# Kernel optimization log

Hardware: AMD Instinct MI355X
Metric: run time of the kernel (lower is better)

The kernel has to match this reference:

```python
import jax, jax.numpy as jnp
import numpy as np

B, T, H, M = 16, 1024, 512, 80
NHEADS, HDIM = 8, H // 8


def _p(key, shape, scale=0.05):
    return scale * jax.random.normal(key, shape, dtype=jnp.float32)


def setup_inputs() -> dict:
    key = jax.random.key(0)
    ks = jax.random.split(key, 20)
    return {
        "encoder_memory": jax.random.normal(ks[0], (B, T, H), dtype=jnp.float32),
        "target_mel": jax.random.normal(ks[1], (B, T, M), dtype=jnp.float32),
        # prenet Linear(mel_dim -> hidden_dim)
        "w_prenet": _p(ks[2], (H, M)), "b_prenet": _p(ks[3], (H,)),
        # MultiheadAttention packed in-proj (3H, H) and out-proj (H, H)
        "in_proj_w": _p(ks[4], (3 * H, H)), "in_proj_b": _p(ks[5], (3 * H,)),
        "out_proj_w": _p(ks[6], (H, H)), "out_proj_b": _p(ks[7], (H,)),
        # 2-layer LSTM (torch gate order i,f,g,o); h0=c0=0 each step so W_hh acts on zeros
        "w_ih0": _p(ks[8], (4 * H, 2 * H)), "w_hh0": _p(ks[9], (4 * H, H)),
        "b_ih0": _p(ks[10], (4 * H,)), "b_hh0": _p(ks[11], (4 * H,)),
        "w_ih1": _p(ks[12], (4 * H, H)), "w_hh1": _p(ks[13], (4 * H, H)),
        "b_ih1": _p(ks[14], (4 * H,)), "b_hh1": _p(ks[15], (4 * H,)),
        # mel projection Linear(hidden_dim -> mel_dim)
        "w_mel": _p(ks[16], (M, H)), "b_mel": _p(ks[17], (M,)),
    }


def _lstm_cell_zero_state(x, w_ih, w_hh, b_ih, b_hh):
    # single step from zero (h, c): the W_hh @ h0 term is exactly zero
    gates = x @ w_ih.T + (b_ih + b_hh)  # (B,T,4H)
    i, f, g, o = jnp.split(gates, 4, axis=-1)
    c = jax.nn.sigmoid(i) * jnp.tanh(g)  # f * c_prev == 0
    return jax.nn.sigmoid(o) * jnp.tanh(c)


def reference(encoder_memory, target_mel, w_prenet, b_prenet,
              in_proj_w, in_proj_b, out_proj_w, out_proj_b,
              w_ih0, w_hh0, b_ih0, b_hh0, w_ih1, w_hh1, b_ih1, b_hh1,
              w_mel, b_mel):
    # teacher forcing: prev_mel at step t is zeros (t=0) else target_mel[:, t-1]
    prev = jnp.concatenate(
        [jnp.zeros((B, 1, M), dtype=target_mel.dtype), target_mel[:, :-1]], axis=1)
    pre = jax.nn.relu(prev @ w_prenet.T + b_prenet)  # (B,T,H); dropout is identity (eval)

    # cross-attention: each step's length-1 query attends over all encoder frames,
    # which vectorizes to standard (no-mask) MHA with queries = pre
    wq, wk, wv = jnp.split(in_proj_w, 3, axis=0)
    bq, bk, bv = jnp.split(in_proj_b, 3, axis=0)
    q = (pre @ wq.T + bq).reshape(B, T, NHEADS, HDIM)
    k = (encoder_memory @ wk.T + bk).reshape(B, T, NHEADS, HDIM)
    v = (encoder_memory @ wv.T + bv).reshape(B, T, NHEADS, HDIM)
    scale = 1.0 / jnp.sqrt(jnp.float32(HDIM))
    scores = jnp.einsum('bqhd,bkhd->bhqk', q * scale, k)  # (B,8,T,T)
    attn = jax.nn.softmax(scores, axis=-1)
    ctx = jnp.einsum('bhqk,bkhd->bqhd', attn, v).reshape(B, T, H)
    attn_out = ctx @ out_proj_w.T + out_proj_b  # (B,T,H)

    dec_in = jnp.concatenate([pre, attn_out], axis=-1)  # (B,T,2H)
    h1 = _lstm_cell_zero_state(dec_in, w_ih0, w_hh0, b_ih0, b_hh0)
    h2 = _lstm_cell_zero_state(h1, w_ih1, w_hh1, b_ih1, b_hh1)
    return h2 @ w_mel.T + b_mel  # (B,T,M)
```

## Files before the change

### kernel.cpp

```cpp
#include <hip/hip_runtime.h>


typedef _Float16 f16;
typedef _Float16 f16x8 __attribute__((ext_vector_type(8)));
typedef _Float16 f16x4 __attribute__((ext_vector_type(4)));
typedef float f32x4 __attribute__((ext_vector_type(4)));

constexpr int B_ = 16, T_ = 1024, H_ = 512, M_ = 80;
constexpr int NH_ = 8, D_ = 64;
constexpr int N_ = B_ * T_;

#define MFMA16(a, b, c) __builtin_amdgcn_mfma_f32_16x16x32_f16(a, b, c, 0, 0, 0)

__device__ __forceinline__ void gload_lds16(const f16* g, f16* l) {
  __builtin_amdgcn_global_load_lds(
      (const __attribute__((address_space(1))) void*)g,
      (__attribute__((address_space(3))) void*)l, 16, 0, 0);
}

template <int EPI, bool CONCATA, bool NCHK>
__global__ __launch_bounds__(256) void mgemm(
    const f16* __restrict__ A, const f16* __restrict__ A2,
    const f16* __restrict__ Wt, const float* __restrict__ bias,
    const float* __restrict__ bias2, float scale, void* __restrict__ outp,
    int K, int N) {
  __shared__ f16 As[128 * 64];
  __shared__ f16 Bs[128 * 64];
  const int tid = threadIdx.x;
  const int lane = tid & 63, wid = tid >> 6;
  const int lq = lane & 15, lg = lane >> 4;
  const int wm = wid >> 1, wn = wid & 1;
  const int r0 = blockIdx.x * 128, c0 = blockIdx.y * 128;

  f32x4 acc[4][4] = {};

  for (int k0 = 0; k0 < K; k0 += 64) {
#pragma unroll
    for (int it = 0; it < 4; ++it) {
      const int off = it * 4096 + wid * 1024 + lane * 16;
      const int row = off >> 7;
      const int cb = (off >> 4) & 7;
      const int kc = k0 + ((cb ^ (row & 7)) << 3);
      const f16* src;
      if (CONCATA) {
        src = (kc < 512) ? (A + (size_t)(r0 + row) * 512 + kc)
                         : (A2 + (size_t)(r0 + row) * 512 + (kc - 512));
      } else {
        src = A + (size_t)(r0 + row) * K + kc;
      }
      gload_lds16(src, (f16*)((char*)As + off));
    }
#pragma unroll
    for (int it = 0; it < 4; ++it) {
      const int off = it * 4096 + wid * 1024 + lane * 16;
      const int row = off >> 7;
      const int cb = (off >> 4) & 7;
      int crow = c0 + row;
      if (NCHK) crow = crow < N ? crow : N - 1;
      gload_lds16(Wt + (size_t)crow * K + k0 + ((cb ^ (row & 7)) << 3),
                  (f16*)((char*)Bs + off));
    }
    __syncthreads();
#pragma unroll
    for (int kk = 0; kk < 2; ++kk) {
      f16x8 af[4], bf[4];
#pragma unroll
      for (int m = 0; m < 4; ++m) {
        const int row = wm * 64 + m * 16 + lq;
        af[m] = *(const f16x8*)((const char*)As + row * 128 +
                                (((kk * 4 + lg) ^ (row & 7)) << 4));
      }
#pragma unroll
      for (int n = 0; n < 4; ++n) {
        const int row = wn * 64 + n * 16 + lq;
        bf[n] = *(const f16x8*)((const char*)Bs + row * 128 +
                                (((kk * 4 + lg) ^ (row & 7)) << 4));
      }
#pragma unroll
      for (int m = 0; m < 4; ++m)
#pragma unroll
        for (int n = 0; n < 4; ++n) acc[m][n] = MFMA16(af[m], bf[n], acc[m][n]);
    }
    __syncthreads();
  }

#pragma unroll
  for (int m = 0; m < 4; ++m) {
    const int rbase = r0 + wm * 64 + m * 16 + lg * 4;
#pragma unroll
    for (int n = 0; n < 4; ++n) {
      const int col = c0 + wn * 64 + n * 16 + lq;
      if (NCHK && col >= N) continue;
      const float bsum = bias[col] + (bias2 ? bias2[col] : 0.f);
      const f32x4 a = acc[m][n];
      if (EPI == 3) {
        const int b = rbase >> 10, t = rbase & (T_ - 1);
        const int head = col >> 6, d = col & 63;
        f16x4 pk;
#pragma unroll
        for (int r = 0; r < 4; ++r) pk[r] = (f16)((a[r] + bsum) * scale);
        *(f16x4*)((f16*)outp + ((size_t)((b * NH_ + head) * D_ + d)) * T_ + t) =
            pk;
      } else {
#pragma unroll
        for (int r = 0; r < 4; ++r) {
          const int row = rbase + r;
          float v = (a[r] + bsum) * scale;
          if (EPI == 1) v = fmaxf(v, 0.f);
          if (EPI == 4)
            ((float*)outp)[(size_t)row * N + col] = v;
          else
            ((f16*)outp)[(size_t)row * N + col] = (f16)v;
        }
      }
    }
  }
}

template <bool CONCATA>
__global__ __launch_bounds__(256, 2) void lstm_fused(
    const f16* __restrict__ A, const f16* __restrict__ A2,
    const f16* __restrict__ Wih, const float* __restrict__ bih,
    const float* __restrict__ bhh, f16* __restrict__ Hout_) {
  constexpr int K = CONCATA ? 1024 : 512;
  __shared__ f16 As[128 * 64];
  __shared__ f16 Bs[3][128 * 64];
  const int tid = threadIdx.x;
  const int lane = tid & 63, wid = tid >> 6;
  const int lq = lane & 15, lg = lane >> 4;
  const int wm = wid >> 1, wn = wid & 1;
  const int r0 = blockIdx.x * 128, c0 = blockIdx.y * 128;

  f32x4 acc[3][4][4] = {};

  for (int k0 = 0; k0 < K; k0 += 64) {
#pragma unroll
    for (int it = 0; it < 4; ++it) {
      const int off = it * 4096 + tid * 16;
      const int row = off >> 7;
      const int cb = (off >> 4) & 7;
      const int kc = k0 + ((cb ^ (row & 7)) << 3);
      const f16* src;
      if (CONCATA) {
        src = (kc < 512) ? (A + (size_t)(r0 + row) * 512 + kc)
                         : (A2 + (size_t)(r0 + row) * 512 + (kc - 512));
      } else {
        src = A + (size_t)(r0 + row) * K + kc;
      }
      gload_lds16(src, (f16*)((char*)As + off));
    }
#pragma unroll
    for (int g = 0; g < 3; ++g) {
      const int gbase = (g == 0) ? 0 : 512 * (g + 1);
#pragma unroll
      for (int it = 0; it < 4; ++it) {
        const int off = it * 4096 + tid * 16;
        const int row = off >> 7;
        const int cb = (off >> 4) & 7;
        gload_lds16(
            Wih + (size_t)(gbase + c0 + row) * K + k0 + ((cb ^ (row & 7)) << 3),
            (f16*)((char*)&Bs[g][0] + off));
      }
    }
    __syncthreads();
#pragma unroll
    for (int kk = 0; kk < 2; ++kk) {
      f16x8 af[4];
#pragma unroll
      for (int m = 0; m < 4; ++m) {
        const int row = wm * 64 + m * 16 + lq;
        af[m] = *(const f16x8*)((const char*)As + row * 128 +
                                (((kk * 4 + lg) ^ (row & 7)) << 4));
      }
#pragma unroll
      for (int g = 0; g < 3; ++g)
#pragma unroll
        for (int n = 0; n < 4; ++n) {
          const int row = wn * 64 + n * 16 + lq;
          const f16x8 bf = *(const f16x8*)((const char*)&Bs[g][0] + row * 128 +
                                           (((kk * 4 + lg) ^ (row & 7)) << 4));
#pragma unroll
          for (int m = 0; m < 4; ++m)
            acc[g][m][n] = MFMA16(af[m], bf, acc[g][m][n]);
        }
    }
    __syncthreads();
  }

#pragma unroll
  for (int n = 0; n < 4; ++n) {
    const int c = c0 + wn * 64 + n * 16 + lq;
    const float bi = bih[c] + bhh[c];
    const float bg = bih[1024 + c] + bhh[1024 + c];
    const float bo = bih[1536 + c] + bhh[1536 + c];
#pragma unroll
    for (int m = 0; m < 4; ++m) {
      const int rbase = r0 + wm * 64 + m * 16 + lg * 4;
#pragma unroll
      for (int r = 0; r < 4; ++r) {
        const float gi = acc[0][m][n][r] + bi;
        const float gg = acc[1][m][n][r] + bg;
        const float go = acc[2][m][n][r] + bo;
        const float si = 1.f / (1.f + __expf(-gi));
        const float so = 1.f / (1.f + __expf(-go));
        const float tg = 2.f / (1.f + __expf(-2.f * gg)) - 1.f;
        const float cc = si * tg;
        const float tc = 2.f / (1.f + __expf(-2.f * cc)) - 1.f;
        Hout_[(size_t)(rbase + r) * 512 + c] = (f16)(so * tc);
      }
    }
  }
}

__global__ __launch_bounds__(256, 2) void kv_fused(
    const f16* __restrict__ A, const f16* __restrict__ Wt,
    const float* __restrict__ bias, f16* __restrict__ kout,
    f16* __restrict__ vout) {
  constexpr int K = 512;
  __shared__ f16 As[128 * 64];
  __shared__ f16 Bs[2][128 * 64];
  const int tid = threadIdx.x;
  const int lane = tid & 63, wid = tid >> 6;
  const int lq = lane & 15, lg = lane >> 4;
  const int wm = wid >> 1, wn = wid & 1;
  const int r0 = blockIdx.x * 128, c0 = blockIdx.y * 128;

  f32x4 acc[2][4][4] = {};

  for (int k0 = 0; k0 < K; k0 += 64) {
#pragma unroll
    for (int it = 0; it < 4; ++it) {
      const int off = it * 4096 + tid * 16;
      const int row = off >> 7;
      const int cb = (off >> 4) & 7;
      const int kc = k0 + ((cb ^ (row & 7)) << 3);
      gload_lds16(A + (size_t)(r0 + row) * K + kc, (f16*)((char*)As + off));
    }
#pragma unroll
    for (int g = 0; g < 2; ++g) {
#pragma unroll
      for (int it = 0; it < 4; ++it) {
        const int off = it * 4096 + tid * 16;
        const int row = off >> 7;
        const int cb = (off >> 4) & 7;
        gload_lds16(
            Wt + (size_t)(g * 512 + c0 + row) * K + k0 + ((cb ^ (row & 7)) << 3),
            (f16*)((char*)&Bs[g][0] + off));
      }
    }
    __syncthreads();
#pragma unroll
    for (int kk = 0; kk < 2; ++kk) {
      f16x8 af[4];
#pragma unroll
      for (int m = 0; m < 4; ++m) {
        const int row = wm * 64 + m * 16 + lq;
        af[m] = *(const f16x8*)((const char*)As + row * 128 +
                                (((kk * 4 + lg) ^ (row & 7)) << 4));
      }
#pragma unroll
      for (int g = 0; g < 2; ++g)
#pragma unroll
        for (int n = 0; n < 4; ++n) {
          const int row = wn * 64 + n * 16 + lq;
          const f16x8 bf = *(const f16x8*)((const char*)&Bs[g][0] + row * 128 +
                                           (((kk * 4 + lg) ^ (row & 7)) << 4));
#pragma unroll
          for (int m = 0; m < 4; ++m)
            acc[g][m][n] = MFMA16(af[m], bf, acc[g][m][n]);
        }
    }
    __syncthreads();
  }

#pragma unroll
  for (int m = 0; m < 4; ++m) {
    const int rbase = r0 + wm * 64 + m * 16 + lg * 4;
    const int b = rbase >> 10, t = rbase & (T_ - 1);
#pragma unroll
    for (int n = 0; n < 4; ++n) {
      const int col = c0 + wn * 64 + n * 16 + lq;
      const float bk = bias[col];
#pragma unroll
      for (int r = 0; r < 4; ++r)
        kout[(size_t)(rbase + r) * 512 + col] = (f16)(acc[0][m][n][r] + bk);
      const float bv = bias[512 + col];
      const int head = col >> 6, d = col & 63;
      f16x4 pk;
#pragma unroll
      for (int r = 0; r < 4; ++r) pk[r] = (f16)(acc[1][m][n][r] + bv);
      *(f16x4*)(vout + ((size_t)((b * NH_ + head) * D_ + d)) * T_ + t) = pk;
    }
  }
}

__global__ __launch_bounds__(256) void attn_mfma3(
    const f16* __restrict__ q, const f16* __restrict__ k,
    const f16* __restrict__ vT, f16* __restrict__ ctx) {
  __shared__ f16 Ks[2][64 * 64];
  __shared__ f16 Vs[2][64 * 64];
  __shared__ f16 Ps[4][16 * 64];
  const int qt = blockIdx.x, head = blockIdx.y, b = blockIdx.z;
  const int tid = threadIdx.x, lane = tid & 63, wid = tid >> 6;
  const int lq = lane & 15, lg = lane >> 4;
  const int bh = b * NH_ + head;

  const f16* kbase = k + ((size_t)b * T_) * H_ + head * D_;
  const f16* vbase = vT + (size_t)bh * D_ * T_;

  auto stage = [&](int kt, int buf) {
#pragma unroll
    for (int it = 0; it < 2; ++it) {
      const int off = it * 4096 + tid * 16;
      const int row = off >> 7;
      const int sc = ((((off >> 4) & 7) ^ (row & 7)) << 3);
      gload_lds16(kbase + (size_t)(kt * 64 + row) * H_ + sc,
                  (f16*)((char*)&Ks[buf][0] + off));
      gload_lds16(vbase + (size_t)row * T_ + kt * 64 + sc,
                  (f16*)((char*)&Vs[buf][0] + off));
    }
  };

  const int q0 = qt * 128 + wid * 32;
  f16x8 qf[2][2];
#pragma unroll
  for (int s = 0; s < 2; ++s)
#pragma unroll
    for (int kk = 0; kk < 2; ++kk)
      qf[s][kk] = *(const f16x8*)(q + ((size_t)(b * T_) + q0 + s * 16 + lq) * H_ +
                                  head * D_ + kk * 32 + lg * 8);

  float m_run[2] = {-1e30f, -1e30f}, l_run[2] = {0.f, 0.f};
  f32x4 accO[2][4] = {};
  char* pw = (char*)&Ps[wid][0] + lq * 128;
  const int psw = (lq & 3) << 5;

  stage(0, 0);
  __syncthreads();

  for (int kt = 0; kt < T_ / 64; ++kt) {
    const int cur = kt & 1;
    if (kt < T_ / 64 - 1) stage(kt + 1, cur ^ 1);

    f16x8 kf[4][2];
#pragma unroll
    for (int n = 0; n < 4; ++n)
#pragma unroll
      for (int kk = 0; kk < 2; ++kk) {
        const int row = n * 16 + lq;
        kf[n][kk] = *(const f16x8*)((const char*)&Ks[cur][0] + row * 128 +
                                    (((kk * 4 + lg) ^ (row & 7)) << 4));
      }
    f32x4 ssw[2][4] = {};
    __builtin_amdgcn_s_setprio(1);
#pragma unroll
    for (int s = 0; s < 2; ++s)
#pragma unroll
      for (int n = 0; n < 4; ++n)
#pragma unroll
        for (int kk = 0; kk < 2; ++kk)
          ssw[s][n] = MFMA16(kf[n][kk], qf[s][kk], ssw[s][n]);
    __builtin_amdgcn_s_setprio(0);

    f16x8 vf[4][2];
#pragma unroll
    for (int n = 0; n < 4; ++n)
#pragma unroll
      for (int kk = 0; kk < 2; ++kk) {
        const int row = n * 16 + lq;
        vf[n][kk] = *(const f16x8*)((const char*)&Vs[cur][0] + row * 128 +
                                    (((kk * 4 + lg) ^ (row & 7)) << 4));
      }

#pragma unroll
    for (int s = 0; s < 2; ++s) {
      float mloc = -1e30f;
#pragma unroll
      for (int n = 0; n < 4; ++n)
#pragma unroll
        for (int r = 0; r < 4; ++r) mloc = fmaxf(mloc, ssw[s][n][r]);
      mloc = fmaxf(mloc, __shfl_xor(mloc, 16, 64));
      mloc = fmaxf(mloc, __shfl_xor(mloc, 32, 64));

      const bool noresc = __all(mloc - m_run[s] <= 8.f);
      if (!noresc) {
        const float nm = fmaxf(m_run[s], mloc);
        const float corr = __expf(m_run[s] - nm);
        m_run[s] = nm;
        l_run[s] *= corr;
#pragma unroll
        for (int n = 0; n < 4; ++n) {
          accO[s][n][0] *= corr; accO[s][n][1] *= corr;
          accO[s][n][2] *= corr; accO[s][n][3] *= corr;
        }
      }
      float sl = 0.f;
#pragma unroll
      for (int n = 0; n < 4; ++n) {
        f16x4 pk;
#pragma unroll
        for (int r = 0; r < 4; ++r) {
          const float p = __expf(ssw[s][n][r] - m_run[s]);
          sl += p;
          pk[r] = (f16)p;
        }
        *(f16x4*)(pw + ((n * 32 + lg * 8) ^ psw)) = pk;
      }
      sl += __shfl_xor(sl, 16, 64);
      sl += __shfl_xor(sl, 32, 64);
      l_run[s] += sl;

      f16x8 pb[2];
#pragma unroll
      for (int kk = 0; kk < 2; ++kk)
        pb[kk] = *(const f16x8*)(pw + ((((kk * 4 + lg) << 4)) ^ psw));
      __builtin_amdgcn_s_setprio(1);
#pragma unroll
      for (int n = 0; n < 4; ++n)
#pragma unroll
        for (int kk = 0; kk < 2; ++kk)
          accO[s][n] = MFMA16(vf[n][kk], pb[kk], accO[s][n]);
      __builtin_amdgcn_s_setprio(0);
    }
    __syncthreads();
  }

#pragma unroll
  for (int s = 0; s < 2; ++s) {
    const float inv = 1.f / l_run[s];
    const size_t rowoff = ((size_t)(b * T_) + q0 + s * 16 + lq) * H_ + head * D_;
#pragma unroll
    for (int n = 0; n < 4; ++n) {
      f16x4 o;
#pragma unroll
      for (int r = 0; r < 4; ++r) o[r] = (f16)(accO[s][n][r] * inv);
      *(f16x4*)(ctx + rowoff + n * 16 + lg * 4) = o;
    }
  }
}

constexpr int C0 = 2097152;
constexpr int C1 = C0 + 196608;
constexpr int C2 = C1 + 65536;
constexpr int C3 = C2 + 524288;
constexpr int C4 = C3 + 262144;
constexpr int C5 = C4 + 10240;
__global__ void conv_all(const float* __restrict__ enc, const float* __restrict__ inw,
                         const float* __restrict__ outw, const float* __restrict__ wih0,
                         const float* __restrict__ wih1, const float* __restrict__ wmel,
                         f16* denc, f16* dinw, f16* doutw, f16* dwih0,
                         f16* dwih1, f16* dwmel) {
  const int i = blockIdx.x * blockDim.x + threadIdx.x;
  const float* s;
  f16* d;
  int off;
  if (i < C0) { s = enc; d = denc; off = i; }
  else if (i < C1) { s = inw; d = dinw; off = i - C0; }
  else if (i < C2) { s = outw; d = doutw; off = i - C1; }
  else if (i < C3) { s = wih0; d = dwih0; off = i - C2; }
  else if (i < C4) { s = wih1; d = dwih1; off = i - C3; }
  else if (i < C5) { s = wmel; d = dwmel; off = i - C4; }
  else return;
  const float4 v = ((const float4*)s)[off];
  f16x4 o = {(f16)v.x, (f16)v.y, (f16)v.z, (f16)v.w};
  ((f16x4*)d)[off] = o;
}

__global__ void build_pm(const float* __restrict__ tmel, f16* __restrict__ pm) {
  const int i = blockIdx.x * blockDim.x + threadIdx.x;
  const int r = i >> 5, c4 = (i & 31) * 4;
  const int t = r & (T_ - 1);
  f16x4 o = {};
  if (t != 0 && c4 < M_) {
    const float4 v = *(const float4*)(tmel + (size_t)(r - 1) * M_ + c4);
    o = {(f16)v.x, (f16)v.y, (f16)v.z, (f16)v.w};
  }
  *(f16x4*)(pm + (size_t)r * 128 + c4) = o;
}

__global__ void build_wp(const float* __restrict__ w, f16* __restrict__ wp) {
  const int i = blockIdx.x * blockDim.x + threadIdx.x;
  const int r = i >> 5, c4 = (i & 31) * 4;
  f16x4 o = {};
  if (c4 < M_) {
    const float4 v = *(const float4*)(w + (size_t)r * M_ + c4);
    o = {(f16)v.x, (f16)v.y, (f16)v.z, (f16)v.w};
  }
  *(f16x4*)(wp + (size_t)r * 128 + c4) = o;
}

extern "C" void kernel_launch(void* const* d_in, const int* in_sizes, int n_in,
                              void* d_out, int out_size, void* d_ws,
                              size_t ws_size, hipStream_t stream) {
  const float* enc = (const float*)d_in[0];
  const float* tmel = (const float*)d_in[1];
  const float* w_pre = (const float*)d_in[2];
  const float* b_pre = (const float*)d_in[3];
  const float* inw = (const float*)d_in[4];
  const float* inb = (const float*)d_in[5];
  const float* outw = (const float*)d_in[6];
  const float* outb = (const float*)d_in[7];
  const float* wih0 = (const float*)d_in[8];
  const float* bih0 = (const float*)d_in[10];
  const float* bhh0 = (const float*)d_in[11];
  const float* wih1 = (const float*)d_in[12];
  const float* bih1 = (const float*)d_in[14];
  const float* bhh1 = (const float*)d_in[15];
  const float* wmel = (const float*)d_in[16];
  const float* bmel = (const float*)d_in[17];

  f16* wsh = (f16*)d_ws;
  const size_t SEG = (size_t)N_ * H_;
  f16* EncB = wsh;
  f16* h1 = wsh + SEG;
  f16* pre = wsh + 2 * SEG;
  f16* qb = wsh + 3 * SEG;
  f16* kbuf = wsh + 4 * SEG;
  f16* vTb = wsh + 5 * SEG;
  f16* ctx = wsh + 6 * SEG;
  f16* aout = EncB;
  f16* h2 = qb;
  f16* WP = wsh + 7 * SEG;
  f16* WIN = WP + 512 * 128;
  f16* WOUT = WIN + 1536 * 512;
  f16* WIH0 = WOUT + 512 * 512;
  f16* WIH1 = WIH0 + 2048 * 1024;
  f16* WMEL = WIH1 + 2048 * 512;
  f16* PM = WMEL + 80 * 512;

  const dim3 blk(256);
  conv_all<<<(C5 + 255) / 256, blk, 0, stream>>>(enc, inw, outw, wih0, wih1,
                                                 wmel, EncB, WIN, WOUT, WIH0,
                                                 WIH1, WMEL);
  build_pm<<<(N_ * 32) / 256, blk, 0, stream>>>(tmel, PM);
  build_wp<<<(512 * 32) / 256, blk, 0, stream>>>(w_pre, WP);

  const dim3 g512(N_ / 128, 4), g80(N_ / 128, 1);
  mgemm<1, false, false><<<g512, blk, 0, stream>>>(PM, nullptr, WP, b_pre,
                                                   nullptr, 1.f, pre, 128, 512);
  mgemm<0, false, false><<<g512, blk, 0, stream>>>(pre, nullptr, WIN, inb,
                                                   nullptr, 0.125f, qb, 512, 512);
  kv_fused<<<g512, blk, 0, stream>>>(EncB, WIN + 512 * 512, inb + 512, kbuf,
                                     vTb);
  attn_mfma3<<<dim3(T_ / 128, NH_, B_), blk, 0, stream>>>(qb, kbuf, vTb, ctx);
  mgemm<0, false, false><<<g512, blk, 0, stream>>>(ctx, nullptr, WOUT, outb,
                                                   nullptr, 1.f, aout, 512, 512);
  lstm_fused<true><<<g512, blk, 0, stream>>>(pre, aout, WIH0, bih0, bhh0, h1);
  lstm_fused<false><<<g512, blk, 0, stream>>>(h1, nullptr, WIH1, bih1, bhh1, h2);
  mgemm<4, false, true><<<g80, blk, 0, stream>>>(h2, nullptr, WMEL, bmel,
                                                 nullptr, 1.f, (float*)d_out,
                                                 512, 80);
}
```

Measured before the change: 285.7 us.

## Enlarge attention query tile, remap blocks for XCD locality, use exp2 softmax

The attention kernel now gives each wave 64 query rows instead of 32, so every block covers 256 queries and each staged K/V tile is reused twice as much. The grid becomes a 1D launch of 512 blocks, remapped so that blocks sharing a (batch, head) land on the same XCD for L2 reuse. The log2(e) factor is folded into the Q projection scale so softmax can use exp2f, and the three input-conversion kernels are merged into one launch. In exchange there are fewer blocks for the GPU, higher register pressure from the larger accumulators, and a change to the P-buffer swizzle.

```diff
diff --git a/kernel.cpp b/kernel.cpp
--- a/kernel.cpp
+++ b/kernel.cpp
@@ -294,16 +294,18 @@
   }
 }
 
-__global__ __launch_bounds__(256) void attn_mfma3(
+__global__ __launch_bounds__(256) void attn_mfma4(
     const f16* __restrict__ q, const f16* __restrict__ k,
     const f16* __restrict__ vT, f16* __restrict__ ctx) {
   __shared__ f16 Ks[2][64 * 64];
   __shared__ f16 Vs[2][64 * 64];
   __shared__ f16 Ps[4][16 * 64];
-  const int qt = blockIdx.x, head = blockIdx.y, b = blockIdx.z;
+  const int bid = blockIdx.x;
+  const int wq = (bid & 7) * 64 + (bid >> 3);
+  const int qt = wq & 3, bh = wq >> 2;
+  const int head = bh & 7, b = bh >> 3;
   const int tid = threadIdx.x, lane = tid & 63, wid = tid >> 6;
   const int lq = lane & 15, lg = lane >> 4;
-  const int bh = b * NH_ + head;
 
   const f16* kbase = k + ((size_t)b * T_) * H_ + head * D_;
   const f16* vbase = vT + (size_t)bh * D_ * T_;
@@ -321,19 +323,20 @@
     }
   };
 
-  const int q0 = qt * 128 + wid * 32;
-  f16x8 qf[2][2];
-#pragma unroll
-  for (int s = 0; s < 2; ++s)
+  const int q0 = qt * 256 + wid * 64;
+  f16x8 qf[4][2];
+#pragma unroll
+  for (int s = 0; s < 4; ++s)
 #pragma unroll
     for (int kk = 0; kk < 2; ++kk)
       qf[s][kk] = *(const f16x8*)(q + ((size_t)(b * T_) + q0 + s * 16 + lq) * H_ +
                                   head * D_ + kk * 32 + lg * 8);
 
-  float m_run[2] = {-1e30f, -1e30f}, l_run[2] = {0.f, 0.f};
-  f32x4 accO[2][4] = {};
+  float m_run[4] = {-1e30f, -1e30f, -1e30f, -1e30f};
+  float l_run[4] = {0.f, 0.f, 0.f, 0.f};
+  f32x4 accO[4][4] = {};
   char* pw = (char*)&Ps[wid][0] + lq * 128;
-  const int psw = (lq & 3) << 5;
+  const int psw = (lq & 7) << 4;
 
   stage(0, 0);
   __syncthreads();
@@ -342,7 +345,7 @@
     const int cur = kt & 1;
     if (kt < T_ / 64 - 1) stage(kt + 1, cur ^ 1);
 
-    f16x8 kf[4][2];
+    f16x8 kf[4][2], vf[4][2];
 #pragma unroll
     for (int n = 0; n < 4; ++n)
 #pragma unroll
@@ -350,42 +353,33 @@
         const int row = n * 16 + lq;
         kf[n][kk] = *(const f16x8*)((const char*)&Ks[cur][0] + row * 128 +
                                     (((kk * 4 + lg) ^ (row & 7)) << 4));
-      }
-    f32x4 ssw[2][4] = {};
-    __builtin_amdgcn_s_setprio(1);
-#pragma unroll
-    for (int s = 0; s < 2; ++s)
-#pragma unroll
-      for (int n = 0; n < 4; ++n)
-#pragma unroll
-        for (int kk = 0; kk < 2; ++kk)
-          ssw[s][n] = MFMA16(kf[n][kk], qf[s][kk], ssw[s][n]);
-    __builtin_amdgcn_s_setprio(0);
-
-    f16x8 vf[4][2];
-#pragma unroll
-    for (int n = 0; n < 4; ++n)
-#pragma unroll
-      for (int kk = 0; kk < 2; ++kk) {
-        const int row = n * 16 + lq;
         vf[n][kk] = *(const f16x8*)((const char*)&Vs[cur][0] + row * 128 +
                                     (((kk * 4 + lg) ^ (row & 7)) << 4));
       }
 
 #pragma unroll
-    for (int s = 0; s < 2; ++s) {
+    for (int s = 0; s < 4; ++s) {
+      f32x4 ssw[4] = {};
+      __builtin_amdgcn_s_setprio(1);
+#pragma unroll
+      for (int n = 0; n < 4; ++n)
+#pragma unroll
+        for (int kk = 0; kk < 2; ++kk)
+          ssw[n] = MFMA16(kf[n][kk], qf[s][kk], ssw[n]);
+      __builtin_amdgcn_s_setprio(0);
+
       float mloc = -1e30f;
 #pragma unroll
       for (int n = 0; n < 4; ++n)
 #pragma unroll
-        for (int r = 0; r < 4; ++r) mloc = fmaxf(mloc, ssw[s][n][r]);
+        for (int r = 0; r < 4; ++r) mloc = fmaxf(mloc, ssw[n][r]);
       mloc = fmaxf(mloc, __shfl_xor(mloc, 16, 64));
       mloc = fmaxf(mloc, __shfl_xor(mloc, 32, 64));
 
       const bool noresc = __all(mloc - m_run[s] <= 8.f);
       if (!noresc) {
         const float nm = fmaxf(m_run[s], mloc);
-        const float corr = __expf(m_run[s] - nm);
+        const float corr = exp2f(m_run[s] - nm);
         m_run[s] = nm;
         l_run[s] *= corr;
 #pragma unroll
@@ -400,7 +394,7 @@
         f16x4 pk;
 #pragma unroll
         for (int r = 0; r < 4; ++r) {
-          const float p = __expf(ssw[s][n][r] - m_run[s]);
+          const float p = exp2f(ssw[n][r] - m_run[s]);
           sl += p;
           pk[r] = (f16)p;
         }
@@ -426,7 +420,7 @@
   }
 
 #pragma unroll
-  for (int s = 0; s < 2; ++s) {
+  for (int s = 0; s < 4; ++s) {
     const float inv = 1.f / l_run[s];
     const size_t rowoff = ((size_t)(b * T_) + q0 + s * 16 + lq) * H_ + head * D_;
 #pragma unroll
@@ -445,48 +439,49 @@
 constexpr int C3 = C2 + 524288;
 constexpr int C4 = C3 + 262144;
 constexpr int C5 = C4 + 10240;
+constexpr int C6 = C5 + 524288;
+constexpr int C7 = C6 + 16384;
 __global__ void conv_all(const float* __restrict__ enc, const float* __restrict__ inw,
                          const float* __restrict__ outw, const float* __restrict__ wih0,
                          const float* __restrict__ wih1, const float* __restrict__ wmel,
+                         const float* __restrict__ tmel, const float* __restrict__ wpre,
                          f16* denc, f16* dinw, f16* doutw, f16* dwih0,
-                         f16* dwih1, f16* dwmel) {
+                         f16* dwih1, f16* dwmel, f16* dpm, f16* dwp) {
   const int i = blockIdx.x * blockDim.x + threadIdx.x;
-  const float* s;
-  f16* d;
-  int off;
-  if (i < C0) { s = enc; d = denc; off = i; }
-  else if (i < C1) { s = inw; d = dinw; off = i - C0; }
-  else if (i < C2) { s = outw; d = doutw; off = i - C1; }
-  else if (i < C3) { s = wih0; d = dwih0; off = i - C2; }
-  else if (i < C4) { s = wih1; d = dwih1; off = i - C3; }
-  else if (i < C5) { s = wmel; d = dwmel; off = i - C4; }
-  else return;
-  const float4 v = ((const float4*)s)[off];
-  f16x4 o = {(f16)v.x, (f16)v.y, (f16)v.z, (f16)v.w};
-  ((f16x4*)d)[off] = o;
-}
-
-__global__ void build_pm(const float* __restrict__ tmel, f16* __restrict__ pm) {
-  const int i = blockIdx.x * blockDim.x + threadIdx.x;
-  const int r = i >> 5, c4 = (i & 31) * 4;
-  const int t = r & (T_ - 1);
-  f16x4 o = {};
-  if (t != 0 && c4 < M_) {
-    const float4 v = *(const float4*)(tmel + (size_t)(r - 1) * M_ + c4);
-    o = {(f16)v.x, (f16)v.y, (f16)v.z, (f16)v.w};
-  }
-  *(f16x4*)(pm + (size_t)r * 128 + c4) = o;
-}
-
-__global__ void build_wp(const float* __restrict__ w, f16* __restrict__ wp) {
-  const int i = blockIdx.x * blockDim.x + threadIdx.x;
-  const int r = i >> 5, c4 = (i & 31) * 4;
-  f16x4 o = {};
-  if (c4 < M_) {
-    const float4 v = *(const float4*)(w + (size_t)r * M_ + c4);
-    o = {(f16)v.x, (f16)v.y, (f16)v.z, (f16)v.w};
-  }
-  *(f16x4*)(wp + (size_t)r * 128 + c4) = o;
+  if (i >= C7) return;
+  if (i < C5) {
+    const float* s;
+    f16* d;
+    int off;
+    if (i < C0) { s = enc; d = denc; off = i; }
+    else if (i < C1) { s = inw; d = dinw; off = i - C0; }
+    else if (i < C2) { s = outw; d = doutw; off = i - C1; }
+    else if (i < C3) { s = wih0; d = dwih0; off = i - C2; }
+    else if (i < C4) { s = wih1; d = dwih1; off = i - C3; }
+    else { s = wmel; d = dwmel; off = i - C4; }
+    const float4 v = ((const float4*)s)[off];
+    f16x4 o = {(f16)v.x, (f16)v.y, (f16)v.z, (f16)v.w};
+    ((f16x4*)d)[off] = o;
+  } else if (i < C6) {
+    const int j = i - C5;
+    const int r = j >> 5, c4 = (j & 31) * 4;
+    const int t = r & (T_ - 1);
+    f16x4 o = {};
+    if (t != 0 && c4 < M_) {
+      const float4 v = *(const float4*)(tmel + (size_t)(r - 1) * M_ + c4);
+      o = {(f16)v.x, (f16)v.y, (f16)v.z, (f16)v.w};
+    }
+    *(f16x4*)(dpm + (size_t)r * 128 + c4) = o;
+  } else {
+    const int j = i - C6;
+    const int r = j >> 5, c4 = (j & 31) * 4;
+    f16x4 o = {};
+    if (c4 < M_) {
+      const float4 v = *(const float4*)(wpre + (size_t)r * M_ + c4);
+      o = {(f16)v.x, (f16)v.y, (f16)v.z, (f16)v.w};
+    }
+    *(f16x4*)(dwp + (size_t)r * 128 + c4) = o;
+  }
 }
 
 extern "C" void kernel_launch(void* const* d_in, const int* in_sizes, int n_in,
@@ -529,20 +524,18 @@
   f16* PM = WMEL + 80 * 512;
 
   const dim3 blk(256);
-  conv_all<<<(C5 + 255) / 256, blk, 0, stream>>>(enc, inw, outw, wih0, wih1,
-                                                 wmel, EncB, WIN, WOUT, WIH0,
-                                                 WIH1, WMEL);
-  build_pm<<<(N_ * 32) / 256, blk, 0, stream>>>(tmel, PM);
-  build_wp<<<(512 * 32) / 256, blk, 0, stream>>>(w_pre, WP);
+  conv_all<<<(C7 + 255) / 256, blk, 0, stream>>>(
+      enc, inw, outw, wih0, wih1, wmel, tmel, w_pre, EncB, WIN, WOUT, WIH0,
+      WIH1, WMEL, PM, WP);
 
   const dim3 g512(N_ / 128, 4), g80(N_ / 128, 1);
   mgemm<1, false, false><<<g512, blk, 0, stream>>>(PM, nullptr, WP, b_pre,
                                                    nullptr, 1.f, pre, 128, 512);
-  mgemm<0, false, false><<<g512, blk, 0, stream>>>(pre, nullptr, WIN, inb,
-                                                   nullptr, 0.125f, qb, 512, 512);
+  mgemm<0, false, false><<<g512, blk, 0, stream>>>(
+      pre, nullptr, WIN, inb, nullptr, 0.125f * 1.44269504088896f, qb, 512, 512);
   kv_fused<<<g512, blk, 0, stream>>>(EncB, WIN + 512 * 512, inb + 512, kbuf,
                                      vTb);
-  attn_mfma3<<<dim3(T_ / 128, NH_, B_), blk, 0, stream>>>(qb, kbuf, vTb, ctx);
+  attn_mfma4<<<dim3(512), blk, 0, stream>>>(qb, kbuf, vTb, ctx);
   mgemm<0, false, false><<<g512, blk, 0, stream>>>(ctx, nullptr, WOUT, outb,
                                                    nullptr, 1.f, aout, 512, 512);
   lstm_fused<true><<<g512, blk, 0, stream>>>(pre, aout, WIH0, bih0, bhh0, h1);
```

After: 316.8 us. +10.9%, slower.
